# Performance work log

Hardware: AMD Instinct MI355X
Metric: run time of the kernel (lower is better)

## Reference

```python
import jax, jax.numpy as jnp
import numpy as np

N = 131072
IN_C1 = 64
MED_C = 64
OUT_C = 64
EPS = 1e-8


def _glorot(key, shape):
    fan_in = shape[0]
    bound = 1.0 / np.sqrt(fan_in)
    return jax.random.uniform(key, shape, jnp.float32, -bound, bound)


def setup_inputs() -> dict:
    key = jax.random.key(0)
    ks = jax.random.split(key, 16)
    inp = {
        "key_value_input": jax.random.normal(ks[0], (N, IN_C1), jnp.float32),
        "query_input": jax.random.normal(ks[1], (N, 7), jnp.float32),
        # Linear params stored as [in, out] (y = x @ W + b)
        "key_W": _glorot(ks[2], (IN_C1, MED_C)), "key_b": jnp.zeros((MED_C,), jnp.float32),
        "value_W": _glorot(ks[3], (IN_C1, MED_C)), "value_b": jnp.zeros((MED_C,), jnp.float32),
        "T_W": _glorot(ks[4], (7, MED_C * MED_C)), "T_b": jnp.zeros((MED_C * MED_C,), jnp.float32),
        "d1_W": _glorot(ks[5], (MED_C, 64)), "d1_b": jnp.zeros((64,), jnp.float32),
        "d2_W": _glorot(ks[6], (64, 32)), "d2_b": jnp.zeros((32,), jnp.float32),
        "d3_W": _glorot(ks[7], (32, OUT_C)), "d3_b": jnp.zeros((OUT_C,), jnp.float32),
        "scale": jnp.float32(1.0),
    }
    return inp


def reference(key_value_input, query_input, key_W, key_b, value_W, value_b,
              T_W, T_b, d1_W, d1_b, d2_W, d2_b, d3_W, d3_b, scale):
    # Per-token hypernetwork: T [N, med_c, med_c]
    T = (query_input @ T_W + T_b).reshape(-1, MED_C, MED_C)
    k = key_value_input @ key_W + key_b              # [N, med_c]
    v = key_value_input @ value_W + value_b          # [N, med_c]
    # query = T @ kv  (batched mat-vec)
    q = jnp.einsum('nij,nj->ni', T, key_value_input)  # [N, med_c]
    att = q * k
    # F.normalize(p=2, dim=-1, eps=1e-8): x / max(||x||_2, eps)
    norm = jnp.linalg.norm(att, axis=-1, keepdims=True)
    att = att / jnp.maximum(norm, EPS)
    v = jax.nn.softmax(v * scale, axis=-1)
    x = att * v
    # small MLP head d
    h = jax.nn.relu(x @ d1_W + d1_b)
    h = jax.nn.relu(h @ d2_W + d2_b)
    return h @ d3_W + d3_b
```

## Files before the change

### kernel.cpp

```cpp
#include <hip/hip_runtime.h>
#include <math.h>

typedef _Float16 f16_t;
typedef __attribute__((ext_vector_type(8))) _Float16 f16x8;
typedef __attribute__((ext_vector_type(4))) float f32x4;

#define NTOK 131072
#define MT   128
#define TPB  128
#define RP16 72
#define OP32 68
#define SLABB 9216

#define OFF_KEY 0
#define OFF_VAL 4096
#define OFF_T   8192
#define OFF_D1  40960
#define OFF_D2  45056
#define OFF_D3  47104
#define WTOT    49152

__device__ __forceinline__ f32x4 mfma1(f16x8 a, f16x8 b, f32x4 c) {
    return __builtin_amdgcn_mfma_f32_16x16x32_f16(a, b, c, 0, 0, 0);
}

#define DPPF(x, C) __int_as_float(__builtin_amdgcn_update_dpp( \
    0, __float_as_int(x), (C), 0xF, 0xF, true))

__device__ __forceinline__ void red16_sum4(f32x4& x) {
#pragma unroll
    for (int e = 0; e < 4; ++e) {
        float v = x[e];
        v += DPPF(v, 0xB1);
        v += DPPF(v, 0x4E);
        v += DPPF(v, 0x141);
        v += DPPF(v, 0x140);
        x[e] = v;
    }
}
__device__ __forceinline__ void red16_max4(f32x4& x) {
#pragma unroll
    for (int e = 0; e < 4; ++e) {
        float v = x[e];
        v = fmaxf(v, DPPF(v, 0xB1));
        v = fmaxf(v, DPPF(v, 0x4E));
        v = fmaxf(v, DPPF(v, 0x141));
        v = fmaxf(v, DPPF(v, 0x140));
        x[e] = v;
    }
}

struct B2 { f16x8 b0, b1; };

__device__ __forceinline__ B2 loadB_lds(const f16_t* __restrict__ b, int c, int l15, int quad) {
    const char* base = (const char*)b;
    int o0 = (16 * c + l15) * 128 + quad * 16;
    int sw = (l15 & 7) << 4;
    B2 r;
    r.b0 = *(const f16x8*)(base + (o0 ^ sw));
    r.b1 = *(const f16x8*)(base + ((o0 + 64) ^ sw));
    return r;
}

#define GEMML(buf, c, a00, a01, a10, a11, acc0, acc1) do {        \
    B2 Bf = loadB_lds((buf), (c), l15, quad);                      \
    acc0 = mfma1(a01, Bf.b1, mfma1(a00, Bf.b0, acc0));             \
    acc1 = mfma1(a11, Bf.b1, mfma1(a10, Bf.b0, acc1));             \
} while (0)

__device__ __forceinline__ void gl_lds16(const void* g, void* l) {
    __builtin_amdgcn_global_load_lds(
        (const __attribute__((address_space(1))) unsigned int*)g,
        (__attribute__((address_space(3))) unsigned int*)l, 16, 0, 0);
}

__device__ __forceinline__ void stage8k(const f16_t* __restrict__ gsrc, f16_t* lbuf, int tid) {
#pragma unroll
    for (int i = 0; i < 4; ++i) {
        int o = (i * TPB + tid) * 16;
        int g = o ^ (((o >> 7) & 7) << 4);
        gl_lds16((const char*)gsrc + g, (char*)lbuf + (o & ~1023));
    }
}
__device__ __forceinline__ void stage4k_r128(const f16_t* __restrict__ gsrc, f16_t* lbuf, int tid) {
#pragma unroll
    for (int i = 0; i < 2; ++i) {
        int o = (i * TPB + tid) * 16;
        int g = o ^ (((o >> 7) & 7) << 4);
        gl_lds16((const char*)gsrc + g, (char*)lbuf + (o & ~1023));
    }
}
__device__ __forceinline__ void stage4k_r64(const f16_t* __restrict__ gsrc, f16_t* lbuf, int tid) {
#pragma unroll
    for (int i = 0; i < 2; ++i) {
        int o = (i * TPB + tid) * 16;
        int g = o ^ (((o >> 7) & 3) << 4);
        gl_lds16((const char*)gsrc + g, (char*)lbuf + (o & ~1023));
    }
}

#define VMW4() asm volatile("s_waitcnt vmcnt(4)" ::: "memory")
#define VMW0() asm volatile("s_waitcnt vmcnt(0)" ::: "memory")
#define BAR()  do { __builtin_amdgcn_s_barrier(); asm volatile("" ::: "memory"); } while (0)

__global__ __launch_bounds__(256)
void prep_w(const float* __restrict__ keyW, const float* __restrict__ valW,
            const float* __restrict__ TW,   const float* __restrict__ TB,
            const float* __restrict__ d1W,  const float* __restrict__ d2W,
            const float* __restrict__ d3W,  f16_t* __restrict__ wsf)
{
    int idx = blockIdx.x * 256 + threadIdx.x;
    if (idx >= WTOT) return;
    float src;
    if (idx < OFF_VAL) {
        int r = idx - OFF_KEY, n = r >> 6, j = r & 63;
        src = keyW[j * 64 + n];
    } else if (idx < OFF_T) {
        int r = idx - OFF_VAL, n = r >> 6, j = r & 63;
        src = valW[j * 64 + n];
    } else if (idx < OFF_D1) {
        int r = idx - OFF_T, p = r >> 12, q = r & 4095;
        src = (p < 7) ? TW[p * 4096 + q] : TB[q];
    } else if (idx < OFF_D2) {
        int r = idx - OFF_D1, n = r >> 6, j = r & 63;
        src = d1W[j * 64 + n];
    } else if (idx < OFF_D3) {
        int r = idx - OFF_D2, n = r >> 6, j = r & 63;
        src = d2W[j * 32 + n];
    } else {
        int r = idx - OFF_D3, n = r >> 5, j = r & 31;
        src = d3W[j * 64 + n];
    }
    wsf[idx] = (f16_t)src;
}

__device__ __forceinline__ void front_rt(
    f16_t* __restrict__ Rf,
    const f16_t* __restrict__ keyb, const f16_t* __restrict__ valb,
    int l15, int quad, int rtb,
    f16x8 a0, f16x8 a1,
    f32x4 q0, f32x4 q1, f32x4 q2, f32x4 q3,
    f32x4 kbv, f32x4 vbv, float sc)
{
    f32x4 k0 = {}, k1 = {}, k2 = {}, k3 = {}, v0 = {}, v1 = {}, v2 = {}, v3 = {};
    { B2 B = loadB_lds(keyb, 0, l15, quad); k0 = mfma1(a1, B.b1, mfma1(a0, B.b0, k0)); }
    { B2 B = loadB_lds(keyb, 1, l15, quad); k1 = mfma1(a1, B.b1, mfma1(a0, B.b0, k1)); }
    { B2 B = loadB_lds(keyb, 2, l15, quad); k2 = mfma1(a1, B.b1, mfma1(a0, B.b0, k2)); }
    { B2 B = loadB_lds(keyb, 3, l15, quad); k3 = mfma1(a1, B.b1, mfma1(a0, B.b0, k3)); }
    { B2 B = loadB_lds(valb, 0, l15, quad); v0 = mfma1(a1, B.b1, mfma1(a0, B.b0, v0)); }
    { B2 B = loadB_lds(valb, 1, l15, quad); v1 = mfma1(a1, B.b1, mfma1(a0, B.b0, v1)); }
    { B2 B = loadB_lds(valb, 2, l15, quad); v2 = mfma1(a1, B.b1, mfma1(a0, B.b0, v2)); }
    { B2 B = loadB_lds(valb, 3, l15, quad); v3 = mfma1(a1, B.b1, mfma1(a0, B.b0, v3)); }

    f32x4 sv0 = (v0 + vbv[0]) * sc;
    f32x4 sv1 = (v1 + vbv[1]) * sc;
    f32x4 sv2 = (v2 + vbv[2]) * sc;
    f32x4 sv3 = (v3 + vbv[3]) * sc;

    f32x4 mx;
#pragma unroll
    for (int e = 0; e < 4; ++e)
        mx[e] = fmaxf(fmaxf(sv0[e], sv1[e]), fmaxf(sv2[e], sv3[e]));
    red16_max4(mx);
#pragma unroll
    for (int e = 0; e < 4; ++e) {
        sv0[e] = __expf(sv0[e] - mx[e]);
        sv1[e] = __expf(sv1[e] - mx[e]);
        sv2[e] = __expf(sv2[e] - mx[e]);
        sv3[e] = __expf(sv3[e] - mx[e]);
    }
    f32x4 se = sv0 + sv1 + sv2 + sv3;
    red16_sum4(se);

    f32x4 at0 = q0 * (k0 + kbv[0]);
    f32x4 at1 = q1 * (k1 + kbv[1]);
    f32x4 at2 = q2 * (k2 + kbv[2]);
    f32x4 at3 = q3 * (k3 + kbv[3]);
    f32x4 nr = at0 * at0 + at1 * at1 + at2 * at2 + at3 * at3;
    red16_sum4(nr);

    f32x4 fac;
#pragma unroll
    for (int e = 0; e < 4; ++e)
        fac[e] = 1.0f / (fmaxf(sqrtf(nr[e]), 1e-8f) * se[e]);

#pragma unroll
    for (int e = 0; e < 4; ++e) {
        f16_t* rr = Rf + (rtb + quad * 4 + e) * RP16 + l15;
        rr[0]  = (f16_t)(at0[e] * sv0[e] * fac[e]);
        rr[16] = (f16_t)(at1[e] * sv1[e] * fac[e]);
        rr[32] = (f16_t)(at2[e] * sv2[e] * fac[e]);
        rr[48] = (f16_t)(at3[e] * sv3[e] * fac[e]);
    }
}

__device__ __forceinline__ void d1_rt(f16_t* __restrict__ Rf, const f16_t* __restrict__ wb,
                                      int l15, int quad, int rtb, f32x4 b1v)
{
    f16x8 x00 = *(const f16x8*)(Rf + (rtb + l15) * RP16 + quad * 8);
    f16x8 x01 = *(const f16x8*)(Rf + (rtb + l15) * RP16 + 32 + quad * 8);
    f16x8 x10 = *(const f16x8*)(Rf + (rtb + 16 + l15) * RP16 + quad * 8);
    f16x8 x11 = *(const f16x8*)(Rf + (rtb + 16 + l15) * RP16 + 32 + quad * 8);
    f32x4 h00 = {}, h01 = {}, h02 = {}, h03 = {};
    f32x4 h10 = {}, h11 = {}, h12 = {}, h13 = {};
    GEMML(wb, 0, x00, x01, x10, x11, h00, h10);
    GEMML(wb, 1, x00, x01, x10, x11, h01, h11);
    GEMML(wb, 2, x00, x01, x10, x11, h02, h12);
    GEMML(wb, 3, x00, x01, x10, x11, h03, h13);
#pragma unroll
    for (int e = 0; e < 4; ++e) {
        f16_t* r0 = Rf + (rtb + quad * 4 + e) * RP16 + l15;
        r0[0]  = (f16_t)fmaxf(h00[e] + b1v[0], 0.f);
        r0[16] = (f16_t)fmaxf(h01[e] + b1v[1], 0.f);
        r0[32] = (f16_t)fmaxf(h02[e] + b1v[2], 0.f);
        r0[48] = (f16_t)fmaxf(h03[e] + b1v[3], 0.f);
        f16_t* r1 = Rf + (rtb + 16 + quad * 4 + e) * RP16 + l15;
        r1[0]  = (f16_t)fmaxf(h10[e] + b1v[0], 0.f);
        r1[16] = (f16_t)fmaxf(h11[e] + b1v[1], 0.f);
        r1[32] = (f16_t)fmaxf(h12[e] + b1v[2], 0.f);
        r1[48] = (f16_t)fmaxf(h13[e] + b1v[3], 0.f);
    }
}

__device__ __forceinline__ void d2_rt(f16_t* __restrict__ Rf, const f16_t* __restrict__ wb,
                                      int l15, int quad, int rtb, float b20, float b21)
{
    f16x8 x00 = *(const f16x8*)(Rf + (rtb + l15) * RP16 + quad * 8);
    f16x8 x01 = *(const f16x8*)(Rf + (rtb + l15) * RP16 + 32 + quad * 8);
    f16x8 x10 = *(const f16x8*)(Rf + (rtb + 16 + l15) * RP16 + quad * 8);
    f16x8 x11 = *(const f16x8*)(Rf + (rtb + 16 + l15) * RP16 + 32 + quad * 8);
    f32x4 g00 = {}, g01 = {}, g10 = {}, g11 = {};
    GEMML(wb, 0, x00, x01, x10, x11, g00, g10);
    GEMML(wb, 1, x00, x01, x10, x11, g01, g11);
#pragma unroll
    for (int e = 0; e < 4; ++e) {
        f16_t* r0 = Rf + (rtb + quad * 4 + e) * RP16 + l15;
        r0[0]  = (f16_t)fmaxf(g00[e] + b20, 0.f);
        r0[16] = (f16_t)fmaxf(g01[e] + b21, 0.f);
        f16_t* r1 = Rf + (rtb + 16 + quad * 4 + e) * RP16 + l15;
        r1[0]  = (f16_t)fmaxf(g10[e] + b20, 0.f);
        r1[16] = (f16_t)fmaxf(g11[e] + b21, 0.f);
    }
}

__device__ __forceinline__ void d3_rt(f16_t* __restrict__ Rf, float* __restrict__ Of,
                                      const char* __restrict__ d3b,
                                      int l15, int quad, int lane, int rtb,
                                      f32x4 b3v, float* __restrict__ obase)
{
    f16x8 a30 = *(const f16x8*)(Rf + (rtb + l15) * RP16 + quad * 8);
    f16x8 a31 = *(const f16x8*)(Rf + (rtb + 16 + l15) * RP16 + quad * 8);
    const int sw3 = ((l15 >> 1) & 3) << 4;
#pragma unroll
    for (int h = 0; h < 2; ++h) {
        const f16x8 a3 = h ? a31 : a30;
#pragma unroll
        for (int c = 0; c < 4; ++c) {
            int o3 = (16 * c + l15) * 64 + quad * 16;
            f16x8 bw = *(const f16x8*)(d3b + (o3 ^ sw3));
            f32x4 z = {};
            f32x4 o = mfma1(a3, bw, z);
#pragma unroll
            for (int e = 0; e < 4; ++e)
                Of[(quad * 4 + e) * OP32 + 16 * c + l15] = o[e] + b3v[c];
        }
#pragma unroll
        for (int i = 0; i < 4; ++i) {
            const int r4 = i * 4 + quad;
            f32x4 v = *(const f32x4*)(Of + r4 * OP32 + l15 * 4);
            *(f32x4*)(obase + rtb * 64 + h * 1024 + i * 256 + lane * 4) = v;
        }
    }
}

__global__ __launch_bounds__(TPB, 2)
void fused_mfma(const float* __restrict__ kv_in, const float* __restrict__ q_in,
                const float* __restrict__ keyB,  const float* __restrict__ valB,
                const float* __restrict__ d1B,   const float* __restrict__ d2B,
                const float* __restrict__ d3B,   const float* __restrict__ scale_p,
                const f16_t* __restrict__ wsf,   float* __restrict__ out)
{
    __shared__ __align__(16) unsigned char Slab[2][SLABB];
    __shared__ __align__(16) f16_t Qs16[MT][8];
    __shared__ __align__(16) f16_t WB[2][4096];

    const int tid  = threadIdx.x;
    const int wv   = tid >> 6, lane = tid & 63;
    const int quad = lane >> 4, l15 = lane & 15;
    const int RB   = wv * 64;
    const long t0  = (long)blockIdx.x * MT;

    f16_t* __restrict__ Rf = (f16_t*)Slab[wv];
    float* __restrict__ Of = (float*)Slab[wv];

    {
        const int r = lane >> 1, half = lane & 1;
#pragma unroll
        for (int s = 0; s < 2; ++s) {
            const float4* p4 = (const float4*)(kv_in + (t0 + RB + s * 32 + r) * 64 + half * 32);
            f16_t* dst = Rf + (s * 32 + r) * RP16 + half * 32;
#pragma unroll
            for (int b = 0; b < 4; ++b) {
                float4 f0 = p4[2 * b], f1 = p4[2 * b + 1];
                f16x8 h;
                h[0] = (f16_t)f0.x; h[1] = (f16_t)f0.y; h[2] = (f16_t)f0.z; h[3] = (f16_t)f0.w;
                h[4] = (f16_t)f1.x; h[5] = (f16_t)f1.y; h[6] = (f16_t)f1.z; h[7] = (f16_t)f1.w;
                *(f16x8*)(dst + 8 * b) = h;
            }
        }
    }
    {
        const float* qp = q_in + (t0 + RB + lane) * 7;
        f16x8 qh;
#pragma unroll
        for (int p = 0; p < 7; ++p) qh[p] = (f16_t)qp[p];
        qh[7] = (f16_t)1.0f;
        *(f16x8*)&Qs16[RB + lane][0] = qh;
    }
    f32x4 kbv, vbv, b1v, b3v;
#pragma unroll
    for (int c = 0; c < 4; ++c) {
        kbv[c] = keyB[16 * c + l15];  vbv[c] = valB[16 * c + l15];
        b1v[c] = d1B[16 * c + l15];   b3v[c] = d3B[16 * c + l15];
    }
    const float b20 = d2B[l15], b21 = d2B[16 + l15];
    const float sc = scale_p[0];

    stage8k(wsf + OFF_T + 0 * 4096, WB[0], tid);
    stage8k(wsf + OFF_T + 1 * 4096, WB[1], tid);

    f16x8 ah00 = *(const f16x8*)(Rf + l15 * RP16 + quad * 8);
    f16x8 ah01 = *(const f16x8*)(Rf + l15 * RP16 + 32 + quad * 8);
    f16x8 ah10 = *(const f16x8*)(Rf + (16 + l15) * RP16 + quad * 8);
    f16x8 ah11 = *(const f16x8*)(Rf + (16 + l15) * RP16 + 32 + quad * 8);
    f16x8 ah20 = *(const f16x8*)(Rf + (32 + l15) * RP16 + quad * 8);
    f16x8 ah21 = *(const f16x8*)(Rf + (32 + l15) * RP16 + 32 + quad * 8);
    f16x8 ah30 = *(const f16x8*)(Rf + (48 + l15) * RP16 + quad * 8);
    f16x8 ah31 = *(const f16x8*)(Rf + (48 + l15) * RP16 + 32 + quad * 8);

    f32x4 q00 = {}, q01 = {}, q02 = {}, q03 = {};
    f32x4 q10 = {}, q11 = {}, q12 = {}, q13 = {};
    f32x4 q20 = {}, q21 = {}, q22 = {}, q23 = {};
    f32x4 q30 = {}, q31 = {}, q32 = {}, q33 = {};
#pragma unroll 1
    for (int p = 0; p < 8; ++p) {
        const f16_t* tb = WB[p & 1];
        VMW4(); BAR();
        f16_t s0 = Qs16[RB + l15][p];
        f16_t s1 = Qs16[RB + 16 + l15][p];
        f16_t s2 = Qs16[RB + 32 + l15][p];
        f16_t s3 = Qs16[RB + 48 + l15][p];
        f16x8 w0 = {s0, s0, s0, s0, s0, s0, s0, s0};
        f16x8 w1 = {s1, s1, s1, s1, s1, s1, s1, s1};
        f16x8 w2 = {s2, s2, s2, s2, s2, s2, s2, s2};
        f16x8 w3 = {s3, s3, s3, s3, s3, s3, s3, s3};
        f16x8 sa00 = ah00 * w0, sa01 = ah01 * w0;
        f16x8 sa10 = ah10 * w1, sa11 = ah11 * w1;
        f16x8 sa20 = ah20 * w2, sa21 = ah21 * w2;
        f16x8 sa30 = ah30 * w3, sa31 = ah31 * w3;
        { B2 B = loadB_lds(tb, 0, l15, quad);
          q00 = mfma1(sa01, B.b1, mfma1(sa00, B.b0, q00));
          q10 = mfma1(sa11, B.b1, mfma1(sa10, B.b0, q10));
          q20 = mfma1(sa21, B.b1, mfma1(sa20, B.b0, q20));
          q30 = mfma1(sa31, B.b1, mfma1(sa30, B.b0, q30)); }
        { B2 B = loadB_lds(tb, 1, l15, quad);
          q01 = mfma1(sa01, B.b1, mfma1(sa00, B.b0, q01));
          q11 = mfma1(sa11, B.b1, mfma1(sa10, B.b0, q11));
          q21 = mfma1(sa21, B.b1, mfma1(sa20, B.b0, q21));
          q31 = mfma1(sa31, B.b1, mfma1(sa30, B.b0, q31)); }
        { B2 B = loadB_lds(tb, 2, l15, quad);
          q02 = mfma1(sa01, B.b1, mfma1(sa00, B.b0, q02));
          q12 = mfma1(sa11, B.b1, mfma1(sa10, B.b0, q12));
          q22 = mfma1(sa21, B.b1, mfma1(sa20, B.b0, q22));
          q32 = mfma1(sa31, B.b1, mfma1(sa30, B.b0, q32)); }
        { B2 B = loadB_lds(tb, 3, l15, quad);
          q03 = mfma1(sa01, B.b1, mfma1(sa00, B.b0, q03));
          q13 = mfma1(sa11, B.b1, mfma1(sa10, B.b0, q13));
          q23 = mfma1(sa21, B.b1, mfma1(sa20, B.b0, q23));
          q33 = mfma1(sa31, B.b1, mfma1(sa30, B.b0, q33)); }
        BAR();
        const f16_t* nsrc = (p < 6) ? (wsf + OFF_T + (p + 2) * 4096)
                                    : ((p == 6) ? (wsf + OFF_KEY) : (wsf + OFF_VAL));
        stage8k(nsrc, WB[p & 1], tid);
    }
    VMW0(); BAR();

    front_rt(Rf, WB[0], WB[1], l15, quad, 0,  ah00, ah01, q00, q01, q02, q03, kbv, vbv, sc);
    front_rt(Rf, WB[0], WB[1], l15, quad, 16, ah10, ah11, q10, q11, q12, q13, kbv, vbv, sc);
    front_rt(Rf, WB[0], WB[1], l15, quad, 32, ah20, ah21, q20, q21, q22, q23, kbv, vbv, sc);
    front_rt(Rf, WB[0], WB[1], l15, quad, 48, ah30, ah31, q30, q31, q32, q33, kbv, vbv, sc);
    BAR();
    stage8k(wsf + OFF_D1, WB[0], tid);
    stage4k_r128(wsf + OFF_D2, WB[1], tid);
    stage4k_r64 (wsf + OFF_D3, WB[1] + 2048, tid);
    VMW0(); BAR();

    d1_rt(Rf, WB[0], l15, quad, 0,  b1v);
    d1_rt(Rf, WB[0], l15, quad, 32, b1v);
    d2_rt(Rf, WB[1], l15, quad, 0,  b20, b21);
    d2_rt(Rf, WB[1], l15, quad, 32, b20, b21);

    float* __restrict__ obase = out + (t0 + RB) * 64;
    const char* d3b = (const char*)(&WB[1][2048]);
    d3_rt(Rf, Of, d3b, l15, quad, lane, 0,  b3v, obase);
    d3_rt(Rf, Of, d3b, l15, quad, lane, 32, b3v, obase);
}

extern "C" void kernel_launch(void* const* d_in, const int* in_sizes, int n_in,
                              void* d_out, int out_size, void* d_ws, size_t ws_size,
                              hipStream_t stream) {
    (void)in_sizes; (void)n_in; (void)out_size; (void)ws_size;
    const float* kv_in = (const float*)d_in[0];
    const float* q_in  = (const float*)d_in[1];
    const float* keyW  = (const float*)d_in[2];
    const float* keyB  = (const float*)d_in[3];
    const float* valW  = (const float*)d_in[4];
    const float* valB  = (const float*)d_in[5];
    const float* TW    = (const float*)d_in[6];
    const float* TB    = (const float*)d_in[7];
    const float* d1W   = (const float*)d_in[8];
    const float* d1B   = (const float*)d_in[9];
    const float* d2W   = (const float*)d_in[10];
    const float* d2B   = (const float*)d_in[11];
    const float* d3W   = (const float*)d_in[12];
    const float* d3B   = (const float*)d_in[13];
    const float* scale = (const float*)d_in[14];
    f16_t* wsf = (f16_t*)d_ws;
    float* outp = (float*)d_out;

    prep_w<<<(WTOT + 255) / 256, 256, 0, stream>>>(keyW, valW, TW, TB, d1W, d2W, d3W, wsf);
    fused_mfma<<<NTOK / MT, TPB, 0, stream>>>(kv_in, q_in, keyB, valB,
                                              d1B, d2B, d3B, scale, wsf, outp);
}
```

Measured before the change: 127.0 us.

## Halve tokens per block to 64 and wait on LDS before barriers

Each block now processes 64 tokens instead of 128: every wave handles 32 rows rather than 64, so the per-wave register accumulators and the LDS slab are halved and the grid doubles. The goal is higher occupancy and more blocks to spread across CUs. The cost is that every block still stages the full set of T and MLP weights, so the weight-staging work per token doubles. Barriers that follow LDS reads now first wait on lgkmcnt(0), which makes ordering before buffer reuse explicit.

```diff
diff --git a/kernel.cpp b/kernel.cpp
--- a/kernel.cpp
+++ b/kernel.cpp
@@ -6,11 +6,11 @@
 typedef __attribute__((ext_vector_type(4))) float f32x4;
 
 #define NTOK 131072
-#define MT   128
+#define MT   64
 #define TPB  128
 #define RP16 72
 #define OP32 68
-#define SLABB 9216
+#define SLABB 4608
 
 #define OFF_KEY 0
 #define OFF_VAL 4096
@@ -102,6 +102,9 @@
 #define VMW4() asm volatile("s_waitcnt vmcnt(4)" ::: "memory")
 #define VMW0() asm volatile("s_waitcnt vmcnt(0)" ::: "memory")
 #define BAR()  do { __builtin_amdgcn_s_barrier(); asm volatile("" ::: "memory"); } while (0)
+#define BARREL() do { asm volatile("s_waitcnt lgkmcnt(0)" ::: "memory"); \
+                      __builtin_amdgcn_s_barrier(); \
+                      asm volatile("" ::: "memory"); } while (0)
 
 __global__ __launch_bounds__(256)
 void prep_w(const float* __restrict__ keyW, const float* __restrict__ valW,
@@ -287,7 +290,7 @@
     const int tid  = threadIdx.x;
     const int wv   = tid >> 6, lane = tid & 63;
     const int quad = lane >> 4, l15 = lane & 15;
-    const int RB   = wv * 64;
+    const int RB   = wv * 32;
     const long t0  = (long)blockIdx.x * MT;
 
     f16_t* __restrict__ Rf = (f16_t*)Slab[wv];
@@ -295,21 +298,18 @@
 
     {
         const int r = lane >> 1, half = lane & 1;
-#pragma unroll
-        for (int s = 0; s < 2; ++s) {
-            const float4* p4 = (const float4*)(kv_in + (t0 + RB + s * 32 + r) * 64 + half * 32);
-            f16_t* dst = Rf + (s * 32 + r) * RP16 + half * 32;
-#pragma unroll
-            for (int b = 0; b < 4; ++b) {
-                float4 f0 = p4[2 * b], f1 = p4[2 * b + 1];
-                f16x8 h;
-                h[0] = (f16_t)f0.x; h[1] = (f16_t)f0.y; h[2] = (f16_t)f0.z; h[3] = (f16_t)f0.w;
-                h[4] = (f16_t)f1.x; h[5] = (f16_t)f1.y; h[6] = (f16_t)f1.z; h[7] = (f16_t)f1.w;
-                *(f16x8*)(dst + 8 * b) = h;
-            }
+        const float4* p4 = (const float4*)(kv_in + (t0 + RB + r) * 64 + half * 32);
+        f16_t* dst = Rf + r * RP16 + half * 32;
+#pragma unroll
+        for (int b = 0; b < 4; ++b) {
+            float4 f0 = p4[2 * b], f1 = p4[2 * b + 1];
+            f16x8 h;
+            h[0] = (f16_t)f0.x; h[1] = (f16_t)f0.y; h[2] = (f16_t)f0.z; h[3] = (f16_t)f0.w;
+            h[4] = (f16_t)f1.x; h[5] = (f16_t)f1.y; h[6] = (f16_t)f1.z; h[7] = (f16_t)f1.w;
+            *(f16x8*)(dst + 8 * b) = h;
         }
     }
-    {
+    if (lane < 32) {
         const float* qp = q_in + (t0 + RB + lane) * 7;
         f16x8 qh;
 #pragma unroll
@@ -333,52 +333,32 @@
     f16x8 ah01 = *(const f16x8*)(Rf + l15 * RP16 + 32 + quad * 8);
     f16x8 ah10 = *(const f16x8*)(Rf + (16 + l15) * RP16 + quad * 8);
     f16x8 ah11 = *(const f16x8*)(Rf + (16 + l15) * RP16 + 32 + quad * 8);
-    f16x8 ah20 = *(const f16x8*)(Rf + (32 + l15) * RP16 + quad * 8);
-    f16x8 ah21 = *(const f16x8*)(Rf + (32 + l15) * RP16 + 32 + quad * 8);
-    f16x8 ah30 = *(const f16x8*)(Rf + (48 + l15) * RP16 + quad * 8);
-    f16x8 ah31 = *(const f16x8*)(Rf + (48 + l15) * RP16 + 32 + quad * 8);
 
     f32x4 q00 = {}, q01 = {}, q02 = {}, q03 = {};
     f32x4 q10 = {}, q11 = {}, q12 = {}, q13 = {};
-    f32x4 q20 = {}, q21 = {}, q22 = {}, q23 = {};
-    f32x4 q30 = {}, q31 = {}, q32 = {}, q33 = {};
 #pragma unroll 1
     for (int p = 0; p < 8; ++p) {
         const f16_t* tb = WB[p & 1];
         VMW4(); BAR();
         f16_t s0 = Qs16[RB + l15][p];
         f16_t s1 = Qs16[RB + 16 + l15][p];
-        f16_t s2 = Qs16[RB + 32 + l15][p];
-        f16_t s3 = Qs16[RB + 48 + l15][p];
         f16x8 w0 = {s0, s0, s0, s0, s0, s0, s0, s0};
         f16x8 w1 = {s1, s1, s1, s1, s1, s1, s1, s1};
-        f16x8 w2 = {s2, s2, s2, s2, s2, s2, s2, s2};
-        f16x8 w3 = {s3, s3, s3, s3, s3, s3, s3, s3};
         f16x8 sa00 = ah00 * w0, sa01 = ah01 * w0;
         f16x8 sa10 = ah10 * w1, sa11 = ah11 * w1;
-        f16x8 sa20 = ah20 * w2, sa21 = ah21 * w2;
-        f16x8 sa30 = ah30 * w3, sa31 = ah31 * w3;
         { B2 B = loadB_lds(tb, 0, l15, quad);
           q00 = mfma1(sa01, B.b1, mfma1(sa00, B.b0, q00));
-          q10 = mfma1(sa11, B.b1, mfma1(sa10, B.b0, q10));
-          q20 = mfma1(sa21, B.b1, mfma1(sa20, B.b0, q20));
-          q30 = mfma1(sa31, B.b1, mfma1(sa30, B.b0, q30)); }
+          q10 = mfma1(sa11, B.b1, mfma1(sa10, B.b0, q10)); }
         { B2 B = loadB_lds(tb, 1, l15, quad);
           q01 = mfma1(sa01, B.b1, mfma1(sa00, B.b0, q01));
-          q11 = mfma1(sa11, B.b1, mfma1(sa10, B.b0, q11));
-          q21 = mfma1(sa21, B.b1, mfma1(sa20, B.b0, q21));
-          q31 = mfma1(sa31, B.b1, mfma1(sa30, B.b0, q31)); }
+          q11 = mfma1(sa11, B.b1, mfma1(sa10, B.b0, q11)); }
         { B2 B = loadB_lds(tb, 2, l15, quad);
           q02 = mfma1(sa01, B.b1, mfma1(sa00, B.b0, q02));
-          q12 = mfma1(sa11, B.b1, mfma1(sa10, B.b0, q12));
-          q22 = mfma1(sa21, B.b1, mfma1(sa20, B.b0, q22));
-          q32 = mfma1(sa31, B.b1, mfma1(sa30, B.b0, q32)); }
+          q12 = mfma1(sa11, B.b1, mfma1(sa10, B.b0, q12)); }
         { B2 B = loadB_lds(tb, 3, l15, quad);
           q03 = mfma1(sa01, B.b1, mfma1(sa00, B.b0, q03));
-          q13 = mfma1(sa11, B.b1, mfma1(sa10, B.b0, q13));
-          q23 = mfma1(sa21, B.b1, mfma1(sa20, B.b0, q23));
-          q33 = mfma1(sa31, B.b1, mfma1(sa30, B.b0, q33)); }
-        BAR();
+          q13 = mfma1(sa11, B.b1, mfma1(sa10, B.b0, q13)); }
+        BARREL();
         const f16_t* nsrc = (p < 6) ? (wsf + OFF_T + (p + 2) * 4096)
                                     : ((p == 6) ? (wsf + OFF_KEY) : (wsf + OFF_VAL));
         stage8k(nsrc, WB[p & 1], tid);
@@ -387,23 +367,18 @@
 
     front_rt(Rf, WB[0], WB[1], l15, quad, 0,  ah00, ah01, q00, q01, q02, q03, kbv, vbv, sc);
     front_rt(Rf, WB[0], WB[1], l15, quad, 16, ah10, ah11, q10, q11, q12, q13, kbv, vbv, sc);
-    front_rt(Rf, WB[0], WB[1], l15, quad, 32, ah20, ah21, q20, q21, q22, q23, kbv, vbv, sc);
-    front_rt(Rf, WB[0], WB[1], l15, quad, 48, ah30, ah31, q30, q31, q32, q33, kbv, vbv, sc);
-    BAR();
+    BARREL();
     stage8k(wsf + OFF_D1, WB[0], tid);
     stage4k_r128(wsf + OFF_D2, WB[1], tid);
     stage4k_r64 (wsf + OFF_D3, WB[1] + 2048, tid);
     VMW0(); BAR();
 
-    d1_rt(Rf, WB[0], l15, quad, 0,  b1v);
-    d1_rt(Rf, WB[0], l15, quad, 32, b1v);
-    d2_rt(Rf, WB[1], l15, quad, 0,  b20, b21);
-    d2_rt(Rf, WB[1], l15, quad, 32, b20, b21);
+    d1_rt(Rf, WB[0], l15, quad, 0, b1v);
+    d2_rt(Rf, WB[1], l15, quad, 0, b20, b21);
 
     float* __restrict__ obase = out + (t0 + RB) * 64;
     const char* d3b = (const char*)(&WB[1][2048]);
-    d3_rt(Rf, Of, d3b, l15, quad, lane, 0,  b3v, obase);
-    d3_rt(Rf, Of, d3b, l15, quad, lane, 32, b3v, obase);
+    d3_rt(Rf, Of, d3b, l15, quad, lane, 0, b3v, obase);
 }
 
 extern "C" void kernel_launch(void* const* d_in, const int* in_sizes, int n_in,
```

New measurement: 135.8 us. +6.9%, slower.
